# Optimization experiments

Hardware: AMD Instinct MI355X
Metric: run time of the kernel (lower is better)

The kernel has to match this reference:

```python
import jax, jax.numpy as jnp
import numpy as np

DIM = 64
NB = 32
LEFT, RIGHT = -1.0, 1.0
EPS_BIN = 0.01
EPS_SLOPE = 0.01


def setup_inputs() -> dict:
    key = jax.random.key(0)
    ks = jax.random.split(key, 10)
    m, cdim, hid = 16384, 64, 100
    x = jax.random.uniform(ks[0], (m, DIM), minval=LEFT + 1e-3, maxval=RIGHT - 1e-3)
    cond = jax.random.normal(ks[1], (m, cdim))
    def dense(k, i, o, scale=1.0):
        return (jax.random.normal(k, (i, o)) * (scale / np.sqrt(i))).astype(jnp.float32)
    inp = dict(
        x=x, cond=cond,
        periodic_mask=jnp.ones((1, DIM), dtype=jnp.int32),
        w_W1=dense(ks[2], cdim, hid), w_b1=jnp.zeros((hid,), jnp.float32),
        w_W2=dense(ks[3], hid, DIM * NB, 0.1), w_b2=jnp.zeros((DIM * NB,), jnp.float32),
        h_W1=dense(ks[4], cdim, hid), h_b1=jnp.zeros((hid,), jnp.float32),
        h_W2=dense(ks[5], hid, DIM * NB, 0.1), h_b2=jnp.zeros((DIM * NB,), jnp.float32),
        s_W1=dense(ks[6], cdim, hid), s_b1=jnp.zeros((hid,), jnp.float32),
        s_W2=dense(ks[7], hid, DIM * (NB + 1), 0.1), s_b2=jnp.zeros((DIM * (NB + 1),), jnp.float32),
    )
    return inp


def _mlp(c, W1, b1, W2, b2):
    return jax.nn.silu(c @ W1 + b1) @ W2 + b2


def _rq_spline(x, w_logit, h_logit, d_raw, periodic_mask):
    # x: [m, dim]; w/h: [m, dim, NB]; d: [m, dim, NB+1]
    widths = EPS_BIN + (1.0 - EPS_BIN * NB) * jax.nn.softmax(w_logit, axis=-1)
    heights = EPS_BIN + (1.0 - EPS_BIN * NB) * jax.nn.softmax(h_logit, axis=-1)
    derivs = EPS_SLOPE + jax.nn.softplus(d_raw)  # [m, dim, NB+1]
    # periodic dims: tie boundary slopes (last == first)
    pm = periodic_mask.astype(bool)  # [1, dim]
    derivs = derivs.at[..., -1].set(jnp.where(pm, derivs[..., 0], derivs[..., -1]))

    span = RIGHT - LEFT
    cw = LEFT + span * jnp.concatenate(
        [jnp.zeros_like(widths[..., :1]), jnp.cumsum(widths, axis=-1)], axis=-1)
    ch = LEFT + span * jnp.concatenate(
        [jnp.zeros_like(heights[..., :1]), jnp.cumsum(heights, axis=-1)], axis=-1)
    cw = cw.at[..., 0].set(LEFT).at[..., -1].set(RIGHT)
    ch = ch.at[..., 0].set(LEFT).at[..., -1].set(RIGHT)
    wk_all = cw[..., 1:] - cw[..., :-1]   # actual bin widths
    hk_all = ch[..., 1:] - ch[..., :-1]   # actual bin heights

    # bin search: number of interior knots <= x
    idx = jnp.sum((x[..., None] >= cw[..., 1:-1]).astype(jnp.int32), axis=-1)
    idx = jnp.clip(idx, 0, NB - 1)[..., None]  # [m, dim, 1]

    gather = lambda a: jnp.take_along_axis(a, idx, axis=-1)[..., 0]
    cwk = gather(cw[..., :-1])
    chk = gather(ch[..., :-1])
    wk = gather(wk_all)
    hk = gather(hk_all)
    dk = gather(derivs[..., :-1])
    dk1 = gather(derivs[..., 1:])

    delta = hk / wk
    theta = (x - cwk) / wk
    t1m = theta * (1.0 - theta)
    denom = delta + (dk1 + dk - 2.0 * delta) * t1m
    y = chk + hk * (delta * theta * theta + dk * t1m) / denom
    deriv = (delta * delta) * (dk1 * theta * theta + 2.0 * delta * t1m
                               + dk * (1.0 - theta) * (1.0 - theta)) / (denom * denom)
    ladJ = jnp.sum(jnp.log(deriv), axis=-1, keepdims=True)  # [m, 1]
    return y, ladJ


def reference(x, cond, periodic_mask, w_W1, w_b1, w_W2, w_b2,
              h_W1, h_b1, h_W2, h_b2, s_W1, s_b1, s_W2, s_b2):
    m = x.shape[0]
    w = _mlp(cond, w_W1, w_b1, w_W2, w_b2).reshape(m, DIM, NB)
    h = _mlp(cond, h_W1, h_b1, h_W2, h_b2).reshape(m, DIM, NB)
    s = _mlp(cond, s_W1, s_b1, s_W2, s_b2).reshape(m, DIM, NB + 1)
    return _rq_spline(x, w, h, s, periodic_mask)
```

## Files before the change

kernel.cpp:

```cpp
#include <hip/hip_runtime.h>
#include <stdint.h>

#define M_TOTAL 16384
#define DIMS    64
#define CDIM    64
#define HID     100
#define ROWS    32
#define LOG2E   1.4426950408889634f
#define LN2     0.6931471805599453f

typedef __bf16 bf16x8 __attribute__((ext_vector_type(8)));
typedef float  f32x4  __attribute__((ext_vector_type(4)));

#define BKG        14
#define CN_STRIDE  (BKG*16*8)
#define DIM_STRIDE (7*CN_STRIDE)
#define W2M_ELEMS  (DIMS*DIM_STRIDE)
#define B2ALL_ELEMS (DIMS*128)
#define W1M_ELEMS  (3*7*8*16*8)
#define B1_ELEMS   (3*112)
#define W2M_OFF   0
#define B2ALL_OFF (W2M_ELEMS*2)
#define W1M_OFF   (B2ALL_OFF + B2ALL_ELEMS*4)
#define B1_OFF    (W1M_OFF + W1M_ELEMS*2)

__device__ __forceinline__ uint16_t f2bf(float f) {
  uint32_t u = __float_as_uint(f);
  return (uint16_t)((u + 0x8000u) >> 16);
}

__global__ void repack_kernel(
    const float* __restrict__ wW2, const float* __restrict__ wb2,
    const float* __restrict__ hW2, const float* __restrict__ hb2,
    const float* __restrict__ sW2, const float* __restrict__ sb2,
    const float* __restrict__ wW1, const float* __restrict__ hW1,
    const float* __restrict__ sW1,
    const float* __restrict__ wb1, const float* __restrict__ hb1,
    const float* __restrict__ sb1,
    uint16_t* __restrict__ W2m, float* __restrict__ b2all,
    uint16_t* __restrict__ W1m, float* __restrict__ b1all)
{
  int i = blockIdx.x * 256 + threadIdx.x;
  if (i < W2M_ELEMS) {
    int j  = i & 7;
    int c  = (i >> 3) & 15;
    int t  = i >> 7;
    int kg = t % BKG;
    int t2 = t / BKG;
    int cn = t2 % 7;
    int d  = t2 / 7;
    int k   = kg*8 + j;
    int col = cn*16 + c;
    float v = 0.f;
    if (k < HID) {
      if (col < 32)      v = wW2[k*2048 + d*32 + col] * LOG2E;
      else if (col < 64) v = hW2[k*2048 + d*32 + (col-32)] * LOG2E;
      else if (col < 97) v = sW2[k*2112 + d*33 + (col-64)];
    }
    W2m[i] = f2bf(v);
    return;
  }
  i -= W2M_ELEMS;
  if (i < B2ALL_ELEMS) {
    int c = i & 127;
    int d = i >> 7;
    float v = 0.f;
    if (c < 32)      v = wb2[d*32 + c] * LOG2E;
    else if (c < 64) v = hb2[d*32 + (c-32)] * LOG2E;
    else if (c < 97) v = sb2[d*33 + (c-64)];
    b2all[i] = v;
    return;
  }
  i -= B2ALL_ELEMS;
  if (i < W1M_ELEMS) {
    int jj = i & 7;
    int c  = (i >> 3) & 15;
    int kg = (i >> 7) & 7;
    int t  = i >> 10;
    int cn = t % 7;
    int mat = t / 7;
    int j = cn*16 + c;
    int k = kg*8 + jj;
    const float* W1 = (mat == 0) ? wW1 : (mat == 1) ? hW1 : sW1;
    W1m[i] = f2bf((j < HID) ? W1[k*HID + j] : 0.f);
    return;
  }
  i -= W1M_ELEMS;
  if (i < B1_ELEMS) {
    int mat = i / 112, col = i % 112;
    const float* b1 = (mat == 0) ? wb1 : (mat == 1) ? hb1 : sb1;
    b1all[i] = (col < HID) ? b1[col] : 0.f;
  }
}

__global__ __launch_bounds__(256, 2)
void spline_main(
    const float* __restrict__ X, const float* __restrict__ C,
    const int* __restrict__ pmask,
    const uint16_t* __restrict__ W2m, const float* __restrict__ b2all,
    const uint16_t* __restrict__ W1m, const float* __restrict__ b1all,
    float* __restrict__ Y, float* __restrict__ LADJ)
{
  __shared__ union {
    float cond_s[ROWS*68];
    float Ls[4][ROWS*100];
  } U;
  __shared__ uint16_t At[3*16*ROWS*8];
  __shared__ float LjLds[4][ROWS];

  const int tid = threadIdx.x;
  const int r0 = blockIdx.x * ROWS;
  const int lane = tid & 63, wv = tid >> 6;
  const int l15 = lane & 15, lkg = lane >> 4;
  const int hb = lane >> 5;
  const int srow = lane & 31;

  for (int i = tid; i < ROWS*CDIM; i += 256) {
    int r = i >> 6, c = i & 63;
    U.cond_s[r*68 + c] = C[(size_t)(r0 + r)*CDIM + c];
  }
  __syncthreads();

  {
    bf16x8 cf[2][2];
#pragma unroll
    for (int m = 0; m < 2; ++m)
#pragma unroll
      for (int ks = 0; ks < 2; ++ks) {
        const float* cp = &U.cond_s[(m*16 + l15)*68 + ks*32 + lkg*8];
        float4 c0 = *(const float4*)cp;
        float4 c1 = *(const float4*)(cp + 4);
        union { uint16_t u[8]; bf16x8 v; } tmp;
        tmp.u[0]=f2bf(c0.x); tmp.u[1]=f2bf(c0.y); tmp.u[2]=f2bf(c0.z); tmp.u[3]=f2bf(c0.w);
        tmp.u[4]=f2bf(c1.x); tmp.u[5]=f2bf(c1.y); tmp.u[6]=f2bf(c1.z); tmp.u[7]=f2bf(c1.w);
        cf[m][ks] = tmp.v;
      }
    for (int t = wv; t < 21; t += 4) {
      int mat = t / 7, cn = t % 7;
      const uint16_t* Wb = W1m + (size_t)(mat*7 + cn)*1024;
      bf16x8 wf[2];
#pragma unroll
      for (int ks = 0; ks < 2; ++ks)
        wf[ks] = *(const bf16x8*)&Wb[(ks*4 + lkg)*128 + l15*8];
      f32x4 h0 = {0.f,0.f,0.f,0.f}, h1 = {0.f,0.f,0.f,0.f};
#pragma unroll
      for (int ks = 0; ks < 2; ++ks) {
        h0 = __builtin_amdgcn_mfma_f32_16x16x32_bf16(cf[0][ks], wf[ks], h0, 0, 0, 0);
        h1 = __builtin_amdgcn_mfma_f32_16x16x32_bf16(cf[1][ks], wf[ks], h1, 0, 0, 0);
      }
      float bb = b1all[mat*112 + cn*16 + l15];
      int j = cn*16 + l15;
      int base = mat*4096 + (j >> 3)*256 + (j & 7);
#pragma unroll
      for (int r = 0; r < 4; ++r) {
        float a0 = h0[r] + bb;
        float v0 = a0 * __builtin_amdgcn_rcpf(1.f + __builtin_amdgcn_exp2f(-LOG2E*a0));
        At[base + (lkg*4 + r)*8] = f2bf(v0);
        float a1 = h1[r] + bb;
        float v1 = a1 * __builtin_amdgcn_rcpf(1.f + __builtin_amdgcn_exp2f(-LOG2E*a1));
        At[base + (16 + lkg*4 + r)*8] = f2bf(v1);
      }
    }
    for (int i2 = tid; i2 < 768; i2 += 256) {
      int mat = i2 >> 8, q = i2 & 255;
      *(uint32_t*)&At[mat*4096 + 14*256 + q*2] = 0u;
    }
  }
  __syncthreads();

  float* LsW = &U.Ls[wv][0];
  const int dbase = wv*16;
  float ladj2 = 0.f;
  float xq = 0.f; int pq = 0;

  auto SPLINE = [&](int d, float xv, int pm) {
    const float* Lr = LsW + srow*100 + hb*32;
    float e[32];
#pragma unroll
    for (int q = 0; q < 8; ++q) *(float4*)&e[4*q] = *(const float4*)(Lr + 4*q);
    float s16[16];
#pragma unroll
    for (int k = 0; k < 16; ++k) s16[k] = e[2*k] + e[2*k+1];
#pragma unroll
    for (int k = 0; k < 8; ++k) s16[k] = s16[2*k] + s16[2*k+1];
#pragma unroll
    for (int k = 0; k < 4; ++k) s16[k] = s16[2*k] + s16[2*k+1];
    float S = (s16[0] + s16[1]) + (s16[2] + s16[3]);
    float rs = __builtin_amdgcn_rcpf(S);
    float Aa = (xv + 1.f) * 0.7352941176470588f * S;
    float Uq = 0.014705882352941176f * S;
    float T = Aa, Pc = 0.f, fidx = 0.f;
#pragma unroll
    for (int c = 1; c <= 31; ++c) {
      Pc += e[c-1]; T -= Uq;
      fidx = (Pc <= T) ? (float)c : fidx;
    }
    float foth = __shfl_xor(fidx, 32);
    float idxu = hb ? foth : fidx;
    float Psel = 0.f, esel = e[0];
#pragma unroll
    for (int c = 0; c < 32; ++c) {
      float cfv = (float)c;
      Psel += (cfv < idxu) ? e[c] : 0.f;
      esel  = (cfv == idxu) ? e[c] : esel;
    }
    float cK = fmaf(0.02f, idxu, -1.f) + 1.36f*rs*Psel;
    float wK = (idxu > 30.5f) ? (1.f - cK) : fmaf(1.36f*rs, esel, 0.02f);
    int idxi = (int)idxu;
    int off = 64 + idxi + hb;
    if (hb && idxi == 31) off = pm ? 64 : 96;
    float sl = LsW[srow*100 + off];
    float dkv = fmaf(LN2, __builtin_amdgcn_logf(1.f + __builtin_amdgcn_exp2f(LOG2E*sl)), 0.01f);
    float cO = __shfl_xor(cK, 32);
    float wO = __shfl_xor(wK, 32);
    float dO = __shfl_xor(dkv, 32);
    float cwk = cK, wk = wK, dk = dkv, chk = cO, hk = wO, dk1 = dO;
    float rw = __builtin_amdgcn_rcpf(wk);
    float th = (xv - cwk)*rw;
    float delta = hk*rw;
    float omt = 1.f - th, t1m = th*omt, th2 = th*th;
    float denom = fmaf(dk1 + dk - 2.f*delta, t1m, delta);
    float rden = __builtin_amdgcn_rcpf(denom);
    float yv = fmaf(hk*fmaf(delta, th2, dk*t1m), rden, chk);
    float dn2 = fmaf(dk1, th2, fmaf(2.f*delta, t1m, dk*omt*omt));
    ladj2 += 2.f*(__builtin_amdgcn_logf(delta) - __builtin_amdgcn_logf(denom))
           + __builtin_amdgcn_logf(dn2);
    if (!hb) Y[(size_t)(r0 + srow)*DIMS + d] = yv;
  };

  auto LOADA = [&](bf16x8 (&a2)[2][4], int mat) {
#pragma unroll
    for (int m = 0; m < 2; ++m)
#pragma unroll
      for (int ks = 0; ks < 4; ++ks)
        a2[m][ks] = *(const bf16x8*)&At[mat*4096 + (ks*4 + lkg)*256 + (m*16 + l15)*8];
  };

  auto DO = [&](const bf16x8 (&afm)[2][4], const bf16x8 (&B)[4],
                float bb, int col, bool doexp) {
    f32x4 a0 = {bb,bb,bb,bb}, a1 = {bb,bb,bb,bb};
#pragma unroll
    for (int ks = 0; ks < 4; ++ks)
      a0 = __builtin_amdgcn_mfma_f32_16x16x32_bf16(afm[0][ks], B[ks], a0, 0, 0, 0);
#pragma unroll
    for (int ks = 0; ks < 4; ++ks)
      a1 = __builtin_amdgcn_mfma_f32_16x16x32_bf16(afm[1][ks], B[ks], a1, 0, 0, 0);
    if (doexp) {
#pragma unroll
      for (int r = 0; r < 4; ++r) {
        a0[r] = __builtin_amdgcn_exp2f(a0[r]);
        a1[r] = __builtin_amdgcn_exp2f(a1[r]);
      }
    }
    if (col < 97) {
#pragma unroll
      for (int r = 0; r < 4; ++r) {
        LsW[(lkg*4 + r)*100 + col]      = a0[r];
        LsW[(16 + lkg*4 + r)*100 + col] = a1[r];
      }
    }
  };

#pragma unroll 1
  for (int dd = 0; dd < 16; ++dd) {
    const int d = dbase + dd;
    const uint16_t* Bd = W2m + (size_t)d*DIM_STRIDE;
    auto LOADB = [&](bf16x8 (&dst)[4], int cn) {
#pragma unroll
      for (int ks = 0; ks < 4; ++ks) {
        int kgb = ks*4 + lkg; kgb = (kgb > 13) ? 13 : kgb;
        dst[ks] = *(const bf16x8*)&Bd[cn*CN_STRIDE + kgb*128 + l15*8];
      }
    };
    bf16x8 bA[4], bB[4], bC[4];
    LOADB(bA, 0); LOADB(bB, 1); LOADB(bC, 2);
    float bbv[7];
#pragma unroll
    for (int cn = 0; cn < 7; ++cn) bbv[cn] = b2all[d*128 + cn*16 + l15];
    float xn = X[(size_t)(r0 + srow)*DIMS + d];
    int pn = pmask[d];

    if (dd > 0) SPLINE(d - 1, xq, pq);
    xq = xn; pq = pn;

    bf16x8 afc[2][4];
    LOADA(afc, 0);
    DO(afc, bA, bbv[0], 0*16 + l15, true);  LOADB(bA, 3);
    DO(afc, bB, bbv[1], 1*16 + l15, true);  LOADB(bB, 4);
    LOADA(afc, 1);
    DO(afc, bC, bbv[2], 2*16 + l15, true);  LOADB(bC, 5);
    DO(afc, bA, bbv[3], 3*16 + l15, true);  LOADB(bA, 6);
    LOADA(afc, 2);
    DO(afc, bB, bbv[4], 4*16 + l15, false);
    DO(afc, bC, bbv[5], 5*16 + l15, false);
    DO(afc, bA, bbv[6], 6*16 + l15, false);
  }
  SPLINE(dbase + 15, xq, pq);

  if (!hb) LjLds[wv][srow] = ladj2;
  __syncthreads();
  if (tid < ROWS)
    LADJ[r0 + tid] = LN2 * ((LjLds[0][tid] + LjLds[1][tid]) + (LjLds[2][tid] + LjLds[3][tid]));
}

extern "C" void kernel_launch(void* const* d_in, const int* in_sizes, int n_in,
                              void* d_out, int out_size, void* d_ws, size_t ws_size,
                              hipStream_t stream) {
  const float* x     = (const float*)d_in[0];
  const float* cond  = (const float*)d_in[1];
  const int*   pmask = (const int*)d_in[2];
  const float* wW1 = (const float*)d_in[3];
  const float* wb1 = (const float*)d_in[4];
  const float* wW2 = (const float*)d_in[5];
  const float* wb2 = (const float*)d_in[6];
  const float* hW1 = (const float*)d_in[7];
  const float* hb1 = (const float*)d_in[8];
  const float* hW2 = (const float*)d_in[9];
  const float* hb2 = (const float*)d_in[10];
  const float* sW1 = (const float*)d_in[11];
  const float* sb1 = (const float*)d_in[12];
  const float* sW2 = (const float*)d_in[13];
  const float* sb2 = (const float*)d_in[14];

  uint16_t* W2m   = (uint16_t*)((char*)d_ws + W2M_OFF);
  float*    b2all = (float*)((char*)d_ws + B2ALL_OFF);
  uint16_t* W1m   = (uint16_t*)((char*)d_ws + W1M_OFF);
  float*    b1all = (float*)((char*)d_ws + B1_OFF);

  const int total = W2M_ELEMS + B2ALL_ELEMS + W1M_ELEMS + B1_ELEMS;
  repack_kernel<<<(total + 255)/256, 256, 0, stream>>>(
      wW2, wb2, hW2, hb2, sW2, sb2, wW1, hW1, sW1, wb1, hb1, sb1,
      W2m, b2all, W1m, b1all);

  float* Y = (float*)d_out;
  float* LADJ = Y + (size_t)M_TOTAL*DIMS;
  spline_main<<<M_TOTAL/ROWS, 256, 0, stream>>>(
      x, cond, pmask, W2m, b2all, W1m, b1all, Y, LADJ);
}
```

Baseline: 64.72 us.

## Split dims across two blocks per row group, shrink LDS, reorder spline phases

Each row group is now handled by two blocks, each covering half of the 64 dims, which doubles the grid. Partial log-det sums go to a workspace and a new small reduce kernel adds them. LDS use drops: the At tile loses its zero-padded k-groups and the logits buffer is narrowed to 66 columns, with the widths/heights region reused for the slopes. This lets launch bounds rise to 3 blocks per SM. The spline is split so the bin search runs between the MFMA phases and the slope evaluation is deferred to the next iteration. The cost is recomputing the first-layer MLP in both blocks and an extra kernel launch.

```diff
diff --git a/kernel.cpp b/kernel.cpp
--- a/kernel.cpp
+++ b/kernel.cpp
@@ -6,6 +6,7 @@
 #define CDIM    64
 #define HID     100
 #define ROWS    32
+#define LS_S    66
 #define LOG2E   1.4426950408889634f
 #define LN2     0.6931471805599453f
 
@@ -23,6 +24,7 @@
 #define B2ALL_OFF (W2M_ELEMS*2)
 #define W1M_OFF   (B2ALL_OFF + B2ALL_ELEMS*4)
 #define B1_OFF    (W1M_OFF + W1M_ELEMS*2)
+#define PART_OFF  1682944
 
 __device__ __forceinline__ uint16_t f2bf(float f) {
   uint32_t u = __float_as_uint(f);
@@ -93,23 +95,30 @@
   }
 }
 
-__global__ __launch_bounds__(256, 2)
+__global__ void ladj_reduce(const float* __restrict__ part, float* __restrict__ LADJ) {
+  int i = blockIdx.x * 256 + threadIdx.x;
+  if (i < M_TOTAL) LADJ[i] = LN2 * (part[i] + part[M_TOTAL + i]);
+}
+
+__global__ __launch_bounds__(256, 3)
 void spline_main(
     const float* __restrict__ X, const float* __restrict__ C,
     const int* __restrict__ pmask,
     const uint16_t* __restrict__ W2m, const float* __restrict__ b2all,
     const uint16_t* __restrict__ W1m, const float* __restrict__ b1all,
-    float* __restrict__ Y, float* __restrict__ LADJ)
+    float* __restrict__ Y, float* __restrict__ part)
 {
   __shared__ union {
     float cond_s[ROWS*68];
-    float Ls[4][ROWS*100];
+    float Ls[4][ROWS*LS_S];
   } U;
-  __shared__ uint16_t At[3*16*ROWS*8];
+  __shared__ uint16_t At[3*13*ROWS*8];
   __shared__ float LjLds[4][ROWS];
 
   const int tid = threadIdx.x;
-  const int r0 = blockIdx.x * ROWS;
+  const int rg = blockIdx.x >> 1;
+  const int dhalf = blockIdx.x & 1;
+  const int r0 = rg * ROWS;
   const int lane = tid & 63, wv = tid >> 6;
   const int l15 = lane & 15, lkg = lane >> 4;
   const int hb = lane >> 5;
@@ -150,31 +159,30 @@
       }
       float bb = b1all[mat*112 + cn*16 + l15];
       int j = cn*16 + l15;
-      int base = mat*4096 + (j >> 3)*256 + (j & 7);
-#pragma unroll
-      for (int r = 0; r < 4; ++r) {
-        float a0 = h0[r] + bb;
-        float v0 = a0 * __builtin_amdgcn_rcpf(1.f + __builtin_amdgcn_exp2f(-LOG2E*a0));
-        At[base + (lkg*4 + r)*8] = f2bf(v0);
-        float a1 = h1[r] + bb;
-        float v1 = a1 * __builtin_amdgcn_rcpf(1.f + __builtin_amdgcn_exp2f(-LOG2E*a1));
-        At[base + (16 + lkg*4 + r)*8] = f2bf(v1);
-      }
-    }
-    for (int i2 = tid; i2 < 768; i2 += 256) {
-      int mat = i2 >> 8, q = i2 & 255;
-      *(uint32_t*)&At[mat*4096 + 14*256 + q*2] = 0u;
+      if ((j >> 3) <= 12) {
+        int base = mat*3328 + (j >> 3)*256 + (j & 7);
+#pragma unroll
+        for (int r = 0; r < 4; ++r) {
+          float a0 = h0[r] + bb;
+          float v0 = a0 * __builtin_amdgcn_rcpf(1.f + __builtin_amdgcn_exp2f(-LOG2E*a0));
+          At[base + (lkg*4 + r)*8] = f2bf(v0);
+          float a1 = h1[r] + bb;
+          float v1 = a1 * __builtin_amdgcn_rcpf(1.f + __builtin_amdgcn_exp2f(-LOG2E*a1));
+          At[base + (16 + lkg*4 + r)*8] = f2bf(v1);
+        }
+      }
     }
   }
   __syncthreads();
 
   float* LsW = &U.Ls[wv][0];
-  const int dbase = wv*16;
+  const int dbase = dhalf*32 + wv*8;
   float ladj2 = 0.f;
-  float xq = 0.f; int pq = 0;
-
-  auto SPLINE = [&](int d, float xv, int pm) {
-    const float* Lr = LsW + srow*100 + hb*32;
+  int   c_off = 0;
+  float c_th2 = 0.f, c_t1m = 0.f, c_omt2 = 0.f, c_delta = 1.f, c_hk = 0.f, c_chk = 0.f;
+
+  auto SPLINE_A = [&](float xv, int pm) {
+    const float* Lr = LsW + srow*LS_S + hb*32;
     float e[32];
 #pragma unroll
     for (int q = 0; q < 8; ++q) *(float4*)&e[4*q] = *(const float4*)(Lr + 4*q);
@@ -206,38 +214,48 @@
     }
     float cK = fmaf(0.02f, idxu, -1.f) + 1.36f*rs*Psel;
     float wK = (idxu > 30.5f) ? (1.f - cK) : fmaf(1.36f*rs, esel, 0.02f);
-    int idxi = (int)idxu;
-    int off = 64 + idxi + hb;
-    if (hb && idxi == 31) off = pm ? 64 : 96;
-    float sl = LsW[srow*100 + off];
-    float dkv = fmaf(LN2, __builtin_amdgcn_logf(1.f + __builtin_amdgcn_exp2f(LOG2E*sl)), 0.01f);
     float cO = __shfl_xor(cK, 32);
     float wO = __shfl_xor(wK, 32);
-    float dO = __shfl_xor(dkv, 32);
-    float cwk = cK, wk = wK, dk = dkv, chk = cO, hk = wO, dk1 = dO;
+    float cwk = cK, wk = wK, chk = cO, hk = wO;
     float rw = __builtin_amdgcn_rcpf(wk);
     float th = (xv - cwk)*rw;
     float delta = hk*rw;
-    float omt = 1.f - th, t1m = th*omt, th2 = th*th;
-    float denom = fmaf(dk1 + dk - 2.f*delta, t1m, delta);
+    float omt = 1.f - th;
+    c_th2 = th*th; c_t1m = th*omt; c_omt2 = omt*omt;
+    c_delta = delta; c_hk = hk; c_chk = chk;
+    int idxi = (int)idxu;
+    int off = idxi + hb;
+    if (hb && idxi == 31) off = pm ? 0 : 32;
+    c_off = off;
+    ladj2 += 2.f*__builtin_amdgcn_logf(delta);
+  };
+
+  auto SPLINE_B = [&](int d) {
+    float sl = LsW[srow*LS_S + c_off];
+    float dkv = fmaf(LN2, __builtin_amdgcn_logf(1.f + __builtin_amdgcn_exp2f(LOG2E*sl)), 0.01f);
+    float dO = __shfl_xor(dkv, 32);
+    float dk = dkv, dk1 = dO;
+    float denom = fmaf(dk1 + dk - 2.f*c_delta, c_t1m, c_delta);
     float rden = __builtin_amdgcn_rcpf(denom);
-    float yv = fmaf(hk*fmaf(delta, th2, dk*t1m), rden, chk);
-    float dn2 = fmaf(dk1, th2, fmaf(2.f*delta, t1m, dk*omt*omt));
-    ladj2 += 2.f*(__builtin_amdgcn_logf(delta) - __builtin_amdgcn_logf(denom))
-           + __builtin_amdgcn_logf(dn2);
+    float yv = fmaf(c_hk*fmaf(c_delta, c_th2, dk*c_t1m), rden, c_chk);
+    float dn2 = fmaf(dk1, c_th2, fmaf(2.f*c_delta, c_t1m, dk*c_omt2));
+    ladj2 += __builtin_amdgcn_logf(dn2) - 2.f*__builtin_amdgcn_logf(denom);
     if (!hb) Y[(size_t)(r0 + srow)*DIMS + d] = yv;
   };
 
   auto LOADA = [&](bf16x8 (&a2)[2][4], int mat) {
-#pragma unroll
-    for (int m = 0; m < 2; ++m)
-#pragma unroll
-      for (int ks = 0; ks < 4; ++ks)
-        a2[m][ks] = *(const bf16x8*)&At[mat*4096 + (ks*4 + lkg)*256 + (m*16 + l15)*8];
+    const uint16_t* base = &At[mat*3328];
+#pragma unroll
+    for (int m = 0; m < 2; ++m) {
+#pragma unroll
+      for (int ks = 0; ks < 3; ++ks)
+        a2[m][ks] = *(const bf16x8*)&base[(ks*4 + lkg)*256 + (m*16 + l15)*8];
+      a2[m][3] = *(const bf16x8*)&base[12*256 + (m*16 + l15)*8];
+    }
   };
 
   auto DO = [&](const bf16x8 (&afm)[2][4], const bf16x8 (&B)[4],
-                float bb, int col, bool doexp) {
+                float bb, int scol, bool doexp, bool guard) {
     f32x4 a0 = {bb,bb,bb,bb}, a1 = {bb,bb,bb,bb};
 #pragma unroll
     for (int ks = 0; ks < 4; ++ks)
@@ -252,17 +270,17 @@
         a1[r] = __builtin_amdgcn_exp2f(a1[r]);
       }
     }
-    if (col < 97) {
+    if (!guard || scol < 33) {
 #pragma unroll
       for (int r = 0; r < 4; ++r) {
-        LsW[(lkg*4 + r)*100 + col]      = a0[r];
-        LsW[(16 + lkg*4 + r)*100 + col] = a1[r];
+        LsW[(lkg*4 + r)*LS_S + scol]      = a0[r];
+        LsW[(16 + lkg*4 + r)*LS_S + scol] = a1[r];
       }
     }
   };
 
 #pragma unroll 1
-  for (int dd = 0; dd < 16; ++dd) {
+  for (int dd = 0; dd < 8; ++dd) {
     const int d = dbase + dd;
     const uint16_t* Bd = W2m + (size_t)d*DIM_STRIDE;
     auto LOADB = [&](bf16x8 (&dst)[4], int cn) {
@@ -277,30 +295,33 @@
     float bbv[7];
 #pragma unroll
     for (int cn = 0; cn < 7; ++cn) bbv[cn] = b2all[d*128 + cn*16 + l15];
-    float xn = X[(size_t)(r0 + srow)*DIMS + d];
-    int pn = pmask[d];
-
-    if (dd > 0) SPLINE(d - 1, xq, pq);
-    xq = xn; pq = pn;
+    float xv = X[(size_t)(r0 + srow)*DIMS + d];
+    int pm = pmask[d];
+
+    if (dd > 0) SPLINE_B(d - 1);
 
     bf16x8 afc[2][4];
     LOADA(afc, 0);
-    DO(afc, bA, bbv[0], 0*16 + l15, true);  LOADB(bA, 3);
-    DO(afc, bB, bbv[1], 1*16 + l15, true);  LOADB(bB, 4);
+    DO(afc, bA, bbv[0],  0 + l15, true, false);  LOADB(bA, 3);
+    DO(afc, bB, bbv[1], 16 + l15, true, false);  LOADB(bB, 4);
     LOADA(afc, 1);
-    DO(afc, bC, bbv[2], 2*16 + l15, true);  LOADB(bC, 5);
-    DO(afc, bA, bbv[3], 3*16 + l15, true);  LOADB(bA, 6);
+    DO(afc, bC, bbv[2], 32 + l15, true, false);  LOADB(bC, 5);
+    DO(afc, bA, bbv[3], 48 + l15, true, false);  LOADB(bA, 6);
+
+    SPLINE_A(xv, pm);
+
     LOADA(afc, 2);
-    DO(afc, bB, bbv[4], 4*16 + l15, false);
-    DO(afc, bC, bbv[5], 5*16 + l15, false);
-    DO(afc, bA, bbv[6], 6*16 + l15, false);
-  }
-  SPLINE(dbase + 15, xq, pq);
+    DO(afc, bB, bbv[4],  0 + l15, false, true);
+    DO(afc, bC, bbv[5], 16 + l15, false, true);
+    DO(afc, bA, bbv[6], 32 + l15, false, true);
+  }
+  SPLINE_B(dbase + 7);
 
   if (!hb) LjLds[wv][srow] = ladj2;
   __syncthreads();
   if (tid < ROWS)
-    LADJ[r0 + tid] = LN2 * ((LjLds[0][tid] + LjLds[1][tid]) + (LjLds[2][tid] + LjLds[3][tid]));
+    part[dhalf*M_TOTAL + r0 + tid] =
+      (LjLds[0][tid] + LjLds[1][tid]) + (LjLds[2][tid] + LjLds[3][tid]);
 }
 
 extern "C" void kernel_launch(void* const* d_in, const int* in_sizes, int n_in,
@@ -326,6 +347,7 @@
   float*    b2all = (float*)((char*)d_ws + B2ALL_OFF);
   uint16_t* W1m   = (uint16_t*)((char*)d_ws + W1M_OFF);
   float*    b1all = (float*)((char*)d_ws + B1_OFF);
+  float*    partp = (float*)((char*)d_ws + PART_OFF);
 
   const int total = W2M_ELEMS + B2ALL_ELEMS + W1M_ELEMS + B1_ELEMS;
   repack_kernel<<<(total + 255)/256, 256, 0, stream>>>(
@@ -334,6 +356,7 @@
 
   float* Y = (float*)d_out;
   float* LADJ = Y + (size_t)M_TOTAL*DIMS;
-  spline_main<<<M_TOTAL/ROWS, 256, 0, stream>>>(
-      x, cond, pmask, W2m, b2all, W1m, b1all, Y, LADJ);
-}
+  spline_main<<<(M_TOTAL/ROWS)*2, 256, 0, stream>>>(
+      x, cond, pmask, W2m, b2all, W1m, b1all, Y, partp);
+  ladj_reduce<<<(M_TOTAL + 255)/256, 256, 0, stream>>>(partp, LADJ);
+}
```

Result: slower. 91.56 us (+41.5%).
